# Kernel optimization log

Measured on AMD Instinct MI355X. Metric: run time of the kernel, lower is better.

## Reference

```python
import jax, jax.numpy as jnp
import numpy as np

D_MODEL = 512
NUM_HEADS = 8
HEAD_DIM = D_MODEL // NUM_HEADS  # 64
B, L = 8, 1024


def setup_inputs() -> dict:
    key = jax.random.key(0)
    ks = jax.random.split(key, 6)
    scale = 1.0 / np.sqrt(D_MODEL)
    return {
        "x": jax.random.normal(ks[0], (B, L, D_MODEL), dtype=jnp.float32),
        "mask": jax.random.normal(ks[1], (L, L), dtype=jnp.float32),
        "Wqkv": jax.random.normal(ks[2], (D_MODEL, 3 * D_MODEL), dtype=jnp.float32) * scale,
        "bqkv": jax.random.normal(ks[3], (3 * D_MODEL,), dtype=jnp.float32) * 0.01,
        "Wo": jax.random.normal(ks[4], (D_MODEL, D_MODEL), dtype=jnp.float32) * scale,
        "bo": jax.random.normal(ks[5], (D_MODEL,), dtype=jnp.float32) * 0.01,
    }


def reference(x, mask, Wqkv, bqkv, Wo, bo):
    b, l, _ = x.shape
    qkv = x @ Wqkv + bqkv                                   # [B, L, 3*D]
    # Faithful to torch: reshape to [B, L, H, 3*head_dim] then chunk last dim.
    qkv = qkv.reshape(b, l, NUM_HEADS, 3 * HEAD_DIM)
    qkv = jnp.transpose(qkv, (0, 2, 1, 3))                  # [B, H, L, 3*hd]
    q, k, v = jnp.split(qkv, 3, axis=-1)                    # each [B, H, L, hd]
    scaled = jnp.einsum("bhqd,bhkd->bhqk", q, k) / np.sqrt(HEAD_DIM)
    scaled = scaled + mask                                  # mask broadcasts over [B, H]
    attn = jax.nn.softmax(scaled, axis=-1)
    out = jnp.einsum("bhqk,bhkd->bhqd", attn, v)            # [B, H, L, hd]
    out = jnp.transpose(out, (0, 2, 1, 3)).reshape(b, l, D_MODEL)
    return out @ Wo + bo
```

## Files before the change

### kernel.cpp

```cpp
#include <hip/hip_runtime.h>
#include <hip/hip_bf16.h>
#include <stdint.h>

#define B_ 8
#define L_ 1024
#define DM 512
#define H_ 8
#define HD 64
#define N3 1536
#define M_T (B_*L_)
#define LOG2E 1.44269504f

typedef __attribute__((ext_vector_type(8))) short short8;
typedef __attribute__((ext_vector_type(4))) float f32x4;
typedef __attribute__((ext_vector_type(4))) float float4_t;
typedef __attribute__((ext_vector_type(4))) unsigned short ushort4_t;

#define MFMA16(a,b,c) __builtin_amdgcn_mfma_f32_16x16x32_bf16((a),(b),(c),0,0,0)

__device__ __forceinline__ short f2bf(float f){
  union { float f; unsigned u; } v; v.f = f;
  unsigned r = v.u + 0x7fffu + ((v.u >> 16) & 1u);
  return (short)(r >> 16);
}

__device__ __forceinline__ short f2bf_fast(float f){
  __hip_bfloat16 h = __float2bfloat16(f);
  short s; __builtin_memcpy(&s, &h, 2); return s;
}

__global__ __launch_bounds__(256) void k_cvt(const float* __restrict__ x,
                                             short* __restrict__ xb, int n8){
  int i = blockIdx.x*256 + threadIdx.x;
  if (i >= n8) return;
  const float4_t* p = (const float4_t*)x + (size_t)i*2;
  float4_t a = p[0], b = p[1];
  short8 o;
  o[0]=f2bf(a[0]); o[1]=f2bf(a[1]); o[2]=f2bf(a[2]); o[3]=f2bf(a[3]);
  o[4]=f2bf(b[0]); o[5]=f2bf(b[1]); o[6]=f2bf(b[2]); o[7]=f2bf(b[3]);
  *((short8*)xb + i) = o;
}

__global__ __launch_bounds__(256) void k_tr2(const float* __restrict__ W0, short* __restrict__ WT0,
                                             const float* __restrict__ W1, short* __restrict__ WT1){
  __shared__ float t[64][65];
  const float* W; short* WT; int N, n0;
  if (blockIdx.x < 24){ W = W0; WT = WT0; N = N3; n0 = blockIdx.x*64; }
  else                { W = W1; WT = WT1; N = DM; n0 = (blockIdx.x-24)*64; }
  int k0 = blockIdx.y*64;
  int tid = threadIdx.x;
  int r = tid >> 4, c4 = (tid & 15) * 4;
  #pragma unroll
  for (int it=0; it<4; ++it){
    int rr = r + it*16;
    float4_t v = *(const float4_t*)(W + (size_t)(k0+rr)*N + n0 + c4);
    t[rr][c4+0]=v[0]; t[rr][c4+1]=v[1]; t[rr][c4+2]=v[2]; t[rr][c4+3]=v[3];
  }
  __syncthreads();
  #pragma unroll
  for (int it=0; it<4; ++it){
    int n = r + it*16;
    ushort4_t o;
    o[0]=(unsigned short)f2bf(t[c4+0][n]);
    o[1]=(unsigned short)f2bf(t[c4+1][n]);
    o[2]=(unsigned short)f2bf(t[c4+2][n]);
    o[3]=(unsigned short)f2bf(t[c4+3][n]);
    *(ushort4_t*)(WT + (size_t)(n0+n)*DM + k0 + c4) = o;
  }
}

__global__ __launch_bounds__(256) void k_gemm_qkv(
    const short* __restrict__ A, const short* __restrict__ Bt,
    const float* __restrict__ bias,
    short* __restrict__ Qo, short* __restrict__ Ko, short* __restrict__ VTo)
{
  __shared__ __align__(16) short As[2][128*40];
  __shared__ __align__(16) short Bs[2][128*40];
  const int m0 = blockIdx.x*128, n0 = blockIdx.y*128;
  const int tid = threadIdx.x;
  const int w = tid>>6, lane = tid&63, li = lane&15, lg = lane>>4;
  const int wr = (w>>1)*64, wc = (w&1)*64;

  int row[2], seg[2];
  #pragma unroll
  for (int c=0;c<2;++c){ int s = tid + c*256; row[c]=s>>2; seg[c]=s&3; }

  short8 ga[2], gb[2];
  #pragma unroll
  for (int c=0;c<2;++c){
    ga[c] = *(const short8*)(A  + (size_t)(m0+row[c])*DM + seg[c]*8);
    gb[c] = *(const short8*)(Bt + (size_t)(n0+row[c])*DM + seg[c]*8);
  }

  const f32x4 fz = {0.f,0.f,0.f,0.f};
  f32x4 acc[4][4];
  #pragma unroll
  for (int i=0;i<4;++i)
    #pragma unroll
    for (int j=0;j<4;++j) acc[i][j] = fz;

  for (int kt=0; kt<16; ++kt){
    short* as = As[kt&1]; short* bs = Bs[kt&1];
    #pragma unroll
    for (int c=0;c<2;++c){
      *(short8*)&as[row[c]*40 + seg[c]*8] = ga[c];
      *(short8*)&bs[row[c]*40 + seg[c]*8] = gb[c];
    }
    __syncthreads();
    if (kt < 15){
      int k0 = (kt+1)*32;
      #pragma unroll
      for (int c=0;c<2;++c){
        ga[c] = *(const short8*)(A  + (size_t)(m0+row[c])*DM + k0 + seg[c]*8);
        gb[c] = *(const short8*)(Bt + (size_t)(n0+row[c])*DM + k0 + seg[c]*8);
      }
    }
    short8 bfr[4];
    #pragma unroll
    for (int nf=0;nf<4;++nf)
      bfr[nf] = *(const short8*)&bs[(wc + nf*16 + li)*40 + lg*8];
    __builtin_amdgcn_s_setprio(1);
    #pragma unroll
    for (int mf=0;mf<4;++mf){
      short8 af = *(const short8*)&as[(wr + mf*16 + li)*40 + lg*8];
      #pragma unroll
      for (int nf=0;nf<4;++nf)
        acc[mf][nf] = MFMA16(af, bfr[nf], acc[mf][nf]);
    }
    __builtin_amdgcn_s_setprio(0);
    __syncthreads();
  }

  #pragma unroll
  for (int nf=0;nf<4;++nf){
    int n = n0 + wc + nf*16 + li;
    float bv = bias[n];
    unsigned h  = (unsigned)n / 192u;
    unsigned wn = (unsigned)n % 192u;
    unsigned typ = wn >> 6, d = wn & 63u;
    #pragma unroll
    for (int mf=0;mf<4;++mf){
      #pragma unroll
      for (int j=0;j<4;++j){
        int m  = m0 + wr + mf*16 + lg*4 + j;
        int b  = m >> 10, lp = m & 1023;
        size_t bh = (size_t)(b*8 + (int)h);
        float vf = acc[mf][nf][j] + bv;
        if (typ == 0)      Qo [(bh<<16) + ((size_t)lp<<6)  + d]  = f2bf_fast(vf * 0.18033688f);
        else if (typ == 1) Ko [(bh<<16) + ((size_t)lp<<6)  + d]  = f2bf_fast(vf);
        else               VTo[(bh<<16) + ((size_t)d<<10)  + lp] = f2bf_fast(vf);
      }
    }
  }
}

__global__ __launch_bounds__(256) void k_attn(
    const short* __restrict__ Q, const short* __restrict__ Kb,
    const short* __restrict__ VT, const float* __restrict__ mask,
    short* __restrict__ O2)
{
  __shared__ __align__(16) short Ks[64*72];
  __shared__ __align__(16) short Vs[64*72];
  __shared__ __align__(16) short Ps[4][16*72];
  const int bh = blockIdx.y;
  const int q0 = blockIdx.x*64;
  const int tid = threadIdx.x, w = tid>>6, lane = tid&63, li = lane&15, lg = lane>>4;
  const int qw = q0 + w*16;

  const short* Qp = Q  + ((size_t)bh<<16);
  const short* Kp = Kb + ((size_t)bh<<16);
  const short* Vp = VT + ((size_t)bh<<16);

  short8 qf[2];
  #pragma unroll
  for (int t=0;t<2;++t)
    qf[t] = *(const short8*)(Qp + ((size_t)(qw+li)<<6) + t*32 + lg*8);

  short8 ones8;
  #pragma unroll
  for (int e=0;e<8;++e) ones8[e] = (short)0x3f80;

  const f32x4 fz = {0.f,0.f,0.f,0.f};
  f32x4 o[4], osum = fz;
  #pragma unroll
  for (int df=0;df<4;++df) o[df] = fz;

  int srow[2], sseg[2];
  #pragma unroll
  for (int c=0;c<2;++c){ int s = tid + c*256; srow[c]=s>>3; sseg[c]=s&7; }

  short8 gk[2], gv[2];
  #pragma unroll
  for (int c=0;c<2;++c){
    gk[c] = *(const short8*)(Kp + ((size_t)srow[c]<<6)  + sseg[c]*8);
    gv[c] = *(const short8*)(Vp + ((size_t)srow[c]<<10) + sseg[c]*8);
  }

  const float* mbase = mask + (size_t)(qw + lg*4)*1024 + li;

  f32x4 sn[4];
  #pragma unroll
  for (int nf=0;nf<4;++nf)
    #pragma unroll
    for (int j=0;j<4;++j)
      sn[nf][j] = fmaf(mbase[(size_t)j*1024 + nf*16], LOG2E, -17.3123405f);

  short* pw = Ps[w];

  for (int kv0=0; kv0<1024; kv0+=64){
    #pragma unroll
    for (int c=0;c<2;++c){
      *(short8*)&Ks[srow[c]*72 + sseg[c]*8] = gk[c];
      *(short8*)&Vs[srow[c]*72 + sseg[c]*8] = gv[c];
    }
    __syncthreads();

    f32x4 s[4];
    #pragma unroll
    for (int nf=0;nf<4;++nf) s[nf] = sn[nf];

    const bool more = (kv0 < 960);
    float mt[4][4];
    if (more){
      int nx = kv0 + 64;
      #pragma unroll
      for (int c=0;c<2;++c){
        gk[c] = *(const short8*)(Kp + ((size_t)(nx+srow[c])<<6)  + sseg[c]*8);
        gv[c] = *(const short8*)(Vp + ((size_t)srow[c]<<10) + nx + sseg[c]*8);
      }
      #pragma unroll
      for (int nf=0;nf<4;++nf)
        #pragma unroll
        for (int j=0;j<4;++j)
          mt[nf][j] = mbase[(size_t)j*1024 + nx + nf*16];
    }

    __builtin_amdgcn_s_setprio(1);
    #pragma unroll
    for (int nf=0;nf<4;++nf){
      #pragma unroll
      for (int t=0;t<2;++t){
        short8 kf = *(const short8*)&Ks[(nf*16+li)*72 + t*32 + lg*8];
        s[nf] = MFMA16(qf[t], kf, s[nf]);
      }
    }
    __builtin_amdgcn_s_setprio(0);

    #pragma unroll
    for (int nf=0;nf<4;++nf)
      #pragma unroll
      for (int j=0;j<4;++j)
        pw[(lg*4+j)*72 + nf*16 + li] = f2bf_fast(exp2f(s[nf][j]));

    __builtin_amdgcn_s_setprio(1);
    #pragma unroll
    for (int t=0;t<2;++t){
      short8 pf = *(const short8*)&pw[li*72 + t*32 + lg*8];
      osum = MFMA16(pf, ones8, osum);
      #pragma unroll
      for (int df=0;df<4;++df){
        short8 vf = *(const short8*)&Vs[(df*16+li)*72 + t*32 + lg*8];
        o[df] = MFMA16(pf, vf, o[df]);
      }
    }
    __builtin_amdgcn_s_setprio(0);

    if (more){
      #pragma unroll
      for (int nf=0;nf<4;++nf)
        #pragma unroll
        for (int j=0;j<4;++j)
          sn[nf][j] = fmaf(mt[nf][j], LOG2E, -17.3123405f);
    }
    __syncthreads();
  }

  int b = bh >> 3, h = bh & 7;
  float rl[4];
  #pragma unroll
  for (int j=0;j<4;++j) rl[j] = 1.0f / osum[j];
  #pragma unroll
  for (int df=0;df<4;++df)
    #pragma unroll
    for (int j=0;j<4;++j){
      int m   = b*1024 + qw + lg*4 + j;
      int col = h*64 + df*16 + li;
      O2[(size_t)m*512 + col] = f2bf_fast(o[df][j] * rl[j]);
    }
}

__global__ __launch_bounds__(256) void k_gemm_out(
    const short* __restrict__ A, const short* __restrict__ Bt,
    const float* __restrict__ bias, float* __restrict__ out)
{
  __shared__ __align__(16) short As[2][128*40];
  __shared__ __align__(16) short Bs[2][128*40];
  const int m0 = blockIdx.x*128, n0 = blockIdx.y*128;
  const int tid = threadIdx.x;
  const int w = tid>>6, lane = tid&63, li = lane&15, lg = lane>>4;
  const int wr = (w>>1)*64, wc = (w&1)*64;

  int row[2], seg[2];
  #pragma unroll
  for (int c=0;c<2;++c){ int s = tid + c*256; row[c]=s>>2; seg[c]=s&3; }

  short8 ga[2], gb[2];
  #pragma unroll
  for (int c=0;c<2;++c){
    ga[c] = *(const short8*)(A  + (size_t)(m0+row[c])*DM + seg[c]*8);
    gb[c] = *(const short8*)(Bt + (size_t)(n0+row[c])*DM + seg[c]*8);
  }

  const f32x4 fz = {0.f,0.f,0.f,0.f};
  f32x4 acc[4][4];
  #pragma unroll
  for (int i=0;i<4;++i)
    #pragma unroll
    for (int j=0;j<4;++j) acc[i][j] = fz;

  for (int kt=0; kt<16; ++kt){
    short* as = As[kt&1]; short* bs = Bs[kt&1];
    #pragma unroll
    for (int c=0;c<2;++c){
      *(short8*)&as[row[c]*40 + seg[c]*8] = ga[c];
      *(short8*)&bs[row[c]*40 + seg[c]*8] = gb[c];
    }
    __syncthreads();
    if (kt < 15){
      int k0 = (kt+1)*32;
      #pragma unroll
      for (int c=0;c<2;++c){
        ga[c] = *(const short8*)(A  + (size_t)(m0+row[c])*DM + k0 + seg[c]*8);
        gb[c] = *(const short8*)(Bt + (size_t)(n0+row[c])*DM + k0 + seg[c]*8);
      }
    }
    short8 bfr[4];
    #pragma unroll
    for (int nf=0;nf<4;++nf)
      bfr[nf] = *(const short8*)&bs[(wc + nf*16 + li)*40 + lg*8];
    __builtin_amdgcn_s_setprio(1);
    #pragma unroll
    for (int mf=0;mf<4;++mf){
      short8 af = *(const short8*)&as[(wr + mf*16 + li)*40 + lg*8];
      #pragma unroll
      for (int nf=0;nf<4;++nf)
        acc[mf][nf] = MFMA16(af, bfr[nf], acc[mf][nf]);
    }
    __builtin_amdgcn_s_setprio(0);
    __syncthreads();
  }

  #pragma unroll
  for (int nf=0;nf<4;++nf){
    int n = n0 + wc + nf*16 + li;
    float bv = bias[n];
    #pragma unroll
    for (int mf=0;mf<4;++mf){
      #pragma unroll
      for (int j=0;j<4;++j){
        int m = m0 + wr + mf*16 + lg*4 + j;
        out[(size_t)m*DM + n] = acc[mf][nf][j] + bv;
      }
    }
  }
}

extern "C" void kernel_launch(void* const* d_in, const int* in_sizes, int n_in,
                              void* d_out, int out_size, void* d_ws, size_t ws_size,
                              hipStream_t stream)
{
  (void)in_sizes; (void)n_in; (void)out_size; (void)ws_size;
  const float* x    = (const float*)d_in[0];
  const float* mask = (const float*)d_in[1];
  const float* Wqkv = (const float*)d_in[2];
  const float* bqkv = (const float*)d_in[3];
  const float* Wo   = (const float*)d_in[4];
  const float* bo   = (const float*)d_in[5];
  float* out = (float*)d_out;

  short* xb    = (short*)d_ws;
  short* WqkvT = xb    + (size_t)M_T*DM;
  short* WoT   = WqkvT + (size_t)N3*DM;
  short* Qb    = WoT   + (size_t)DM*DM;
  short* Kbf   = Qb    + (size_t)64*1024*64;
  short* VTb   = Kbf   + (size_t)64*1024*64;
  short* O2    = VTb   + (size_t)64*1024*64;

  k_cvt<<<2048, 256, 0, stream>>>(x, xb, (M_T*DM)/8);
  k_tr2<<<dim3(32, 8), 256, 0, stream>>>(Wqkv, WqkvT, Wo, WoT);
  k_gemm_qkv<<<dim3(M_T/128, N3/128), 256, 0, stream>>>(xb, WqkvT, bqkv, Qb, Kbf, VTb);
  k_attn    <<<dim3(L_/64, B_*H_),    256, 0, stream>>>(Qb, Kbf, VTb, mask, O2);
  k_gemm_out<<<dim3(M_T/128, DM/128), 256, 0, stream>>>(O2, WoT, bo, out);
}
```

Measured before the change: 99.68 us.

## Prepack mask in fragment layout, widen attention blocks, double-buffer K/V tiles

A new kernel runs once per call and rewrites the mask into MFMA-fragment order with the log2e scale and offset already applied. It stores the result in the xb workspace, which is free once the QKV GEMM has run. The attention kernel then reads the mask with contiguous float4 loads instead of strided scalar loads and FMA conversion. The attention kernel now uses 512 threads covering 128 queries per block, which halves how often each block reloads K/V. It also double-buffers K/V in LDS with a two-tile-ahead register prefetch, leaving one barrier per iteration. The costs are an extra kernel launch, a 4 MB mask pass on every call, and more LDS per block.

```diff
diff --git a/kernel.cpp b/kernel.cpp
--- a/kernel.cpp
+++ b/kernel.cpp
@@ -67,6 +67,23 @@
     o[3]=(unsigned short)f2bf(t[c4+3][n]);
     *(ushort4_t*)(WT + (size_t)(n0+n)*DM + k0 + c4) = o;
   }
+}
+
+__global__ __launch_bounds__(256) void k_maskp(const float* __restrict__ mask,
+                                               float* __restrict__ maskP){
+  int gid = blockIdx.x*256 + threadIdx.x;
+  int nf  = gid & 3;
+  int lane= (gid>>2) & 63;
+  int kvt = (gid>>8) & 15;
+  int qg  = gid>>12;
+  int li = lane & 15, lg = lane >> 4;
+  int r0 = qg*16 + lg*4;
+  int col = kvt*64 + nf*16 + li;
+  float4_t o;
+  #pragma unroll
+  for (int j=0;j<4;++j)
+    o[j] = fmaf(mask[(size_t)(r0+j)*1024 + col], LOG2E, -17.3123405f);
+  ((float4_t*)maskP)[gid] = o;
 }
 
 __global__ __launch_bounds__(256) void k_gemm_qkv(
@@ -154,16 +171,16 @@
   }
 }
 
-__global__ __launch_bounds__(256) void k_attn(
+__global__ __launch_bounds__(512) void k_attn(
     const short* __restrict__ Q, const short* __restrict__ Kb,
-    const short* __restrict__ VT, const float* __restrict__ mask,
+    const short* __restrict__ VT, const float* __restrict__ maskP,
     short* __restrict__ O2)
 {
-  __shared__ __align__(16) short Ks[64*72];
-  __shared__ __align__(16) short Vs[64*72];
-  __shared__ __align__(16) short Ps[4][16*72];
+  __shared__ __align__(16) short Ks[2][64*72];
+  __shared__ __align__(16) short Vs[2][64*72];
+  __shared__ __align__(16) short Ps[8][16*72];
   const int bh = blockIdx.y;
-  const int q0 = blockIdx.x*64;
+  const int q0 = blockIdx.x*128;
   const int tid = threadIdx.x, w = tid>>6, lane = tid&63, li = lane&15, lg = lane>>4;
   const int qw = q0 + w*16;
 
@@ -185,62 +202,45 @@
   #pragma unroll
   for (int df=0;df<4;++df) o[df] = fz;
 
-  int srow[2], sseg[2];
-  #pragma unroll
-  for (int c=0;c<2;++c){ int s = tid + c*256; srow[c]=s>>3; sseg[c]=s&7; }
-
-  short8 gk[2], gv[2];
-  #pragma unroll
-  for (int c=0;c<2;++c){
-    gk[c] = *(const short8*)(Kp + ((size_t)srow[c]<<6)  + sseg[c]*8);
-    gv[c] = *(const short8*)(Vp + ((size_t)srow[c]<<10) + sseg[c]*8);
-  }
-
-  const float* mbase = mask + (size_t)(qw + lg*4)*1024 + li;
-
-  f32x4 sn[4];
-  #pragma unroll
-  for (int nf=0;nf<4;++nf)
-    #pragma unroll
-    for (int j=0;j<4;++j)
-      sn[nf][j] = fmaf(mbase[(size_t)j*1024 + nf*16], LOG2E, -17.3123405f);
-
+  const int srow = tid>>3, sseg8 = (tid&7)*8;
+
+  short8 gk = *(const short8*)(Kp + ((size_t)srow<<6) + sseg8);
+  short8 gv = *(const short8*)(Vp + ((size_t)srow<<10) + sseg8);
+  *(short8*)&Ks[0][srow*72 + sseg8] = gk;
+  *(short8*)&Vs[0][srow*72 + sseg8] = gv;
+  gk = *(const short8*)(Kp + ((size_t)(64+srow)<<6) + sseg8);
+  gv = *(const short8*)(Vp + ((size_t)srow<<10) + 64 + sseg8);
+  __syncthreads();
+
+  const float* mp0 = maskP + ((size_t)(qw>>4)<<14) + lane*16;
   short* pw = Ps[w];
 
-  for (int kv0=0; kv0<1024; kv0+=64){
-    #pragma unroll
-    for (int c=0;c<2;++c){
-      *(short8*)&Ks[srow[c]*72 + sseg[c]*8] = gk[c];
-      *(short8*)&Vs[srow[c]*72 + sseg[c]*8] = gv[c];
-    }
-    __syncthreads();
-
+  for (int kvt=0; kvt<16; ++kvt){
+    const short* ks = Ks[kvt&1];
+    const short* vs = Vs[kvt&1];
+    if (kvt < 15){
+      short* kd = Ks[(kvt&1)^1]; short* vd = Vs[(kvt&1)^1];
+      *(short8*)&kd[srow*72 + sseg8] = gk;
+      *(short8*)&vd[srow*72 + sseg8] = gv;
+    }
+    if (kvt < 14){
+      int nx = (kvt+2)*64;
+      gk = *(const short8*)(Kp + ((size_t)(nx+srow)<<6) + sseg8);
+      gv = *(const short8*)(Vp + ((size_t)srow<<10) + nx + sseg8);
+    }
+
+    const float* mp = mp0 + (size_t)kvt*1024;
     f32x4 s[4];
     #pragma unroll
-    for (int nf=0;nf<4;++nf) s[nf] = sn[nf];
-
-    const bool more = (kv0 < 960);
-    float mt[4][4];
-    if (more){
-      int nx = kv0 + 64;
-      #pragma unroll
-      for (int c=0;c<2;++c){
-        gk[c] = *(const short8*)(Kp + ((size_t)(nx+srow[c])<<6)  + sseg[c]*8);
-        gv[c] = *(const short8*)(Vp + ((size_t)srow[c]<<10) + nx + sseg[c]*8);
-      }
-      #pragma unroll
-      for (int nf=0;nf<4;++nf)
-        #pragma unroll
-        for (int j=0;j<4;++j)
-          mt[nf][j] = mbase[(size_t)j*1024 + nx + nf*16];
-    }
+    for (int nf=0;nf<4;++nf)
+      s[nf] = *(const float4_t*)(mp + nf*4);
 
     __builtin_amdgcn_s_setprio(1);
     #pragma unroll
     for (int nf=0;nf<4;++nf){
       #pragma unroll
       for (int t=0;t<2;++t){
-        short8 kf = *(const short8*)&Ks[(nf*16+li)*72 + t*32 + lg*8];
+        short8 kf = *(const short8*)&ks[(nf*16+li)*72 + t*32 + lg*8];
         s[nf] = MFMA16(qf[t], kf, s[nf]);
       }
     }
@@ -259,19 +259,12 @@
       osum = MFMA16(pf, ones8, osum);
       #pragma unroll
       for (int df=0;df<4;++df){
-        short8 vf = *(const short8*)&Vs[(df*16+li)*72 + t*32 + lg*8];
+        short8 vf = *(const short8*)&vs[(df*16+li)*72 + t*32 + lg*8];
         o[df] = MFMA16(pf, vf, o[df]);
       }
     }
     __builtin_amdgcn_s_setprio(0);
 
-    if (more){
-      #pragma unroll
-      for (int nf=0;nf<4;++nf)
-        #pragma unroll
-        for (int j=0;j<4;++j)
-          sn[nf][j] = fmaf(mt[nf][j], LOG2E, -17.3123405f);
-    }
     __syncthreads();
   }
 
@@ -385,10 +378,12 @@
   short* Kbf   = Qb    + (size_t)64*1024*64;
   short* VTb   = Kbf   + (size_t)64*1024*64;
   short* O2    = VTb   + (size_t)64*1024*64;
+  float* maskP = (float*)xb;
 
   k_cvt<<<2048, 256, 0, stream>>>(x, xb, (M_T*DM)/8);
   k_tr2<<<dim3(32, 8), 256, 0, stream>>>(Wqkv, WqkvT, Wo, WoT);
   k_gemm_qkv<<<dim3(M_T/128, N3/128), 256, 0, stream>>>(xb, WqkvT, bqkv, Qb, Kbf, VTb);
-  k_attn    <<<dim3(L_/64, B_*H_),    256, 0, stream>>>(Qb, Kbf, VTb, mask, O2);
+  k_maskp<<<1024, 256, 0, stream>>>(mask, maskP);
+  k_attn    <<<dim3(L_/128, B_*H_),   512, 0, stream>>>(Qb, Kbf, VTb, maskP, O2);
   k_gemm_out<<<dim3(M_T/128, DM/128), 256, 0, stream>>>(O2, WoT, bo, out);
 }
```

Result: faster. 93.76 us (-5.9%).
